# Kernel optimization log

Hardware: AMD Instinct MI355X
Metric: run time of the kernel (lower is better)

## Reference

```python
import jax, jax.numpy as jnp
import numpy as np

EMBED_DIM = 1024
NUM_HEADS = 16
D_K = EMBED_DIM // NUM_HEADS
SCALE = D_K ** -0.5
WEIGHT_EPS = 1e-5


def setup_inputs() -> dict:
    key = jax.random.key(0)
    ks = jax.random.split(key, 12)
    B, T, E = 4, 1024, EMBED_DIM
    init = 1.0 / np.sqrt(E)  # ~ nn.Linear default scale
    inp = {
        "q": jax.random.normal(ks[0], (B, T, E), jnp.float32),
        "k": jax.random.normal(ks[1], (B, T, E), jnp.float32),
        "v": jax.random.normal(ks[2], (B, T, E), jnp.float32),
        "weights": jax.random.uniform(ks[3], (B, T), jnp.float32),
        "Wq": jax.random.uniform(ks[4], (E, E), jnp.float32, -init, init),
        "bq": jax.random.uniform(ks[5], (E,), jnp.float32, -init, init),
        "Wk": jax.random.uniform(ks[6], (E, E), jnp.float32, -init, init),
        "bk": jax.random.uniform(ks[7], (E,), jnp.float32, -init, init),
        "Wv": jax.random.uniform(ks[8], (E, E), jnp.float32, -init, init),
        "bv": jax.random.uniform(ks[9], (E,), jnp.float32, -init, init),
        "Wo": jax.random.uniform(ks[10], (E, E), jnp.float32, -init, init),
        "bo": jax.random.uniform(ks[11], (E,), jnp.float32, -init, init),
    }
    return inp


def reference(q, k, v, weights, Wq, bq, Wk, bk, Wv, bv, Wo, bo):
    B, T, E = q.shape
    H, Dk = NUM_HEADS, D_K
    # linear projections (torch Linear: x @ W.T + b), split into heads
    qh = (q @ Wq.T + bq).reshape(B, T, H, Dk).transpose(0, 2, 1, 3)  # [B,H,T,Dk]
    kh = (k @ Wk.T + bk).reshape(B, T, H, Dk).transpose(0, 2, 1, 3)
    vh = (v @ Wv.T + bv).reshape(B, T, H, Dk).transpose(0, 2, 1, 3)
    # scaled energy [B,H,Tq,Tk]
    energy = jnp.einsum("bhqd,bhkd->bhqk", qh, kh) * SCALE
    # weight^2 gating over key axis + masked_fill(-inf) where weight < eps
    w = weights[:, None, None, :]  # [B,1,1,Tk]
    energy = jnp.where(w < WEIGHT_EPS, -jnp.inf, energy * (w * w))
    attn = jax.nn.softmax(energy, axis=-1)  # dropout is identity in eval mode
    out = jnp.einsum("bhqk,bhkd->bhqd", attn, vh)  # [B,H,T,Dk]
    out = out.transpose(0, 2, 1, 3).reshape(B, T, E)
    return out @ Wo.T + bo
```

## Files before the change

### kernel.cpp

```cpp
#include <hip/hip_runtime.h>
#include <hip/hip_bf16.h>
#include <stdint.h>

using frag = __attribute__((ext_vector_type(8))) short;
using f4   = __attribute__((ext_vector_type(4))) float;
using bf16 = __hip_bfloat16;

static constexpr float WEPS = 1e-5f;
static constexpr float SC2K  = 0.125f * 1.44269504f;
static constexpr float EBIAS = -8.0f * 1.44269504f;

#define AS1(p) ((const __attribute__((address_space(1))) void*)(p))
#define AS3(p) ((__attribute__((address_space(3))) void*)(p))

__device__ __forceinline__ void gl2lds16(const void* g, void* l) {
    __builtin_amdgcn_global_load_lds(AS1(g), AS3(l), 16, 0, 0);
}

__device__ inline uint4 pack8(float4 a, float4 b) {
    union { bf16 h[8]; uint4 u; } x;
    x.h[0] = __float2bfloat16(a.x); x.h[1] = __float2bfloat16(a.y);
    x.h[2] = __float2bfloat16(a.z); x.h[3] = __float2bfloat16(a.w);
    x.h[4] = __float2bfloat16(b.x); x.h[5] = __float2bfloat16(b.y);
    x.h[6] = __float2bfloat16(b.z); x.h[7] = __float2bfloat16(b.w);
    return x.u;
}

__device__ __forceinline__ uint2 pack4(float a, float b, float c, float d) {
    union { bf16 h[4]; uint2 u; } x;
    x.h[0] = __float2bfloat16(a); x.h[1] = __float2bfloat16(b);
    x.h[2] = __float2bfloat16(c); x.h[3] = __float2bfloat16(d);
    return x.u;
}

__device__ __forceinline__ int tperm(int t) {
    return (t & ~63) | (((t & 15) << 2) | ((t >> 4) & 3));
}

struct CvtArgs {
    const float* src[7];
    long long    bounds[8];
    long long    total;
};

__global__ __launch_bounds__(256) void cvt_kernel(CvtArgs a, bf16* __restrict__ dst)
{
    long long e = ((long long)blockIdx.x * 256 + threadIdx.x) * 8;
    if (e >= a.total) return;
    int s = 0;
    while (e >= a.bounds[s + 1]) s++;
    const float* src = a.src[s] + (e - a.bounds[s]);
    float4 f0 = ((const float4*)src)[0];
    float4 f1 = ((const float4*)src)[1];
    *(uint4*)(dst + e) = pack8(f0, f1);
}

struct GemmBatch {
    const void*  A[3];
    const void*  W[3];
    const float* bias[3];
    void*        Out[3];
    int          mode[3];
};

template<bool ABF, bool WBF>
__global__ __launch_bounds__(256) void gemm_batch(GemmBatch g)
{
    constexpr int K = 1024;
    __shared__ bf16 As[128 * 32];
    __shared__ bf16 Bs[128 * 32];

    const int z = blockIdx.z;
    const void*  Ap   = g.A[z];
    const void*  Wp   = g.W[z];
    const float* bias = g.bias[z];
    void*        OutP = g.Out[z];
    const int    mode = g.mode[z];

    const int tid  = threadIdx.x;
    int m0, n0;
    if (mode == 4) { m0 = blockIdx.x * 128; n0 = blockIdx.y * 128; }
    else           { n0 = blockIdx.x * 128; m0 = blockIdx.y * 128; }
    const int lane = tid & 63;
    const int wave = tid >> 6;
    const int wm   = (wave >> 1) * 64;
    const int wn   = (wave & 1) * 64;
    const int lr   = lane & 15;
    const int q    = lane >> 4;

    const int sr = tid >> 1;
    const int sc = (tid & 1) * 16;

    const int c0 = wave * 128 + lane;
    const int c1 = c0 + 64;
    const int r0 = c0 >> 2, col0 = (c0 & 3) * 8;
    const int r1 = c1 >> 2, col1 = (c1 & 3) * 8;

    f4 acc[4][4];
    #pragma unroll
    for (int i = 0; i < 4; i++)
        #pragma unroll
        for (int j = 0; j < 4; j++) acc[i][j] = f4{0.f, 0.f, 0.f, 0.f};

    for (int k0 = 0; k0 < K; k0 += 32) {
        if (WBF) {
            const bf16* W = (const bf16*)Wp;
            gl2lds16(&W[(size_t)(n0 + r0) * K + k0 + col0], &Bs[wave * 1024]);
            gl2lds16(&W[(size_t)(n0 + r1) * K + k0 + col1], &Bs[wave * 1024 + 512]);
        } else {
            const float* W = (const float*)Wp;
            const float* src = &W[(size_t)(n0 + sr) * K + k0 + sc];
            float4 f0 = ((const float4*)src)[0];
            float4 f1 = ((const float4*)src)[1];
            float4 f2 = ((const float4*)src)[2];
            float4 f3 = ((const float4*)src)[3];
            *(uint4*)(&Bs[sr * 32 + sc])     = pack8(f0, f1);
            *(uint4*)(&Bs[sr * 32 + sc + 8]) = pack8(f2, f3);
        }
        if (ABF) {
            const bf16* A = (const bf16*)Ap;
            gl2lds16(&A[(size_t)(m0 + r0) * K + k0 + col0], &As[wave * 1024]);
            gl2lds16(&A[(size_t)(m0 + r1) * K + k0 + col1], &As[wave * 1024 + 512]);
        } else {
            const float* A = (const float*)Ap;
            const float* src = &A[(size_t)(m0 + sr) * K + k0 + sc];
            float4 f0 = ((const float4*)src)[0];
            float4 f1 = ((const float4*)src)[1];
            float4 f2 = ((const float4*)src)[2];
            float4 f3 = ((const float4*)src)[3];
            *(uint4*)(&As[sr * 32 + sc])     = pack8(f0, f1);
            *(uint4*)(&As[sr * 32 + sc + 8]) = pack8(f2, f3);
        }
        __syncthreads();

        frag af[4], bfr[4];
        #pragma unroll
        for (int i = 0; i < 4; i++)
            af[i] = *(const frag*)(&As[(wm + i * 16 + lr) * 32 + q * 8]);
        #pragma unroll
        for (int j = 0; j < 4; j++)
            bfr[j] = *(const frag*)(&Bs[(wn + j * 16 + lr) * 32 + q * 8]);
        #pragma unroll
        for (int i = 0; i < 4; i++)
            #pragma unroll
            for (int j = 0; j < 4; j++)
                acc[i][j] = __builtin_amdgcn_mfma_f32_16x16x32_bf16(af[i], bfr[j], acc[i][j], 0, 0, 0);
        __syncthreads();
    }

    #pragma unroll
    for (int i = 0; i < 4; i++) {
        int row0 = m0 + wm + i * 16 + q * 4;
        if (mode == 4) {
            float bvr[4];
            #pragma unroll
            for (int r = 0; r < 4; r++) bvr[r] = bias[row0 + r];
            #pragma unroll
            for (int j = 0; j < 4; j++) {
                int tok = n0 + wn + j * 16 + lr;
                int bbt = tok >> 10, tt = tperm(tok & 1023);
                #pragma unroll
                for (int r = 0; r < 4; r++) {
                    int f = row0 + r;
                    int h = f >> 6, d = f & 63;
                    float val = acc[i][j][r] + bvr[r];
                    ((bf16*)OutP)[((((size_t)bbt * 16 + h) * 64 + d) << 10) + tt] = __float2bfloat16(val);
                }
            }
        } else {
            #pragma unroll
            for (int j = 0; j < 4; j++) {
                int col = n0 + wn + j * 16 + lr;
                float bv = bias[col];
                #pragma unroll
                for (int r = 0; r < 4; r++) {
                    float val = acc[i][j][r] + bv;
                    int mrow = row0 + r;
                    if (mode == 3) {
                        ((float*)OutP)[(size_t)mrow * 1024 + col] = val;
                    } else {
                        int bb = mrow >> 10, t = mrow & 1023;
                        int h  = col >> 6,   d = col & 63;
                        size_t idx;
                        if (mode == 2)
                            idx = ((((size_t)bb * 16 + h) * 64 + d) << 10) + tperm(t);
                        else
                            idx = ((((size_t)bb * 16 + h) << 10) + t) * 64 + d;
                        ((bf16*)OutP)[idx] = __float2bfloat16(val);
                    }
                }
            }
        }
    }
}

template<bool WBF>
__global__ __launch_bounds__(256) void gemm_out(const bf16* __restrict__ A,
                                                const void* __restrict__ Wp,
                                                const float* __restrict__ bias,
                                                float* __restrict__ Out)
{
    constexpr int K = 1024;
    __shared__ bf16 As[64 * 32];
    __shared__ bf16 Bs[128 * 32];

    const int tid  = threadIdx.x;
    const int n0   = blockIdx.x * 128;
    const int m0   = blockIdx.y * 64;
    const int lane = tid & 63;
    const int wave = tid >> 6;
    const int wm   = (wave >> 1) * 32;
    const int wn   = (wave & 1) * 64;
    const int lr   = lane & 15;
    const int q    = lane >> 4;

    const int sr = tid >> 1;
    const int sc = (tid & 1) * 16;

    const int c0 = wave * 128 + lane;
    const int c1 = c0 + 64;
    const int r0 = c0 >> 2, col0 = (c0 & 3) * 8;
    const int r1 = c1 >> 2, col1 = (c1 & 3) * 8;
    const int ca = wave * 64 + lane;
    const int ra = ca >> 2, cola = (ca & 3) * 8;

    f4 acc[2][4];
    #pragma unroll
    for (int i = 0; i < 2; i++)
        #pragma unroll
        for (int j = 0; j < 4; j++) acc[i][j] = f4{0.f, 0.f, 0.f, 0.f};

    for (int k0 = 0; k0 < K; k0 += 32) {
        if (WBF) {
            const bf16* W = (const bf16*)Wp;
            gl2lds16(&W[(size_t)(n0 + r0) * K + k0 + col0], &Bs[wave * 1024]);
            gl2lds16(&W[(size_t)(n0 + r1) * K + k0 + col1], &Bs[wave * 1024 + 512]);
        } else {
            const float* W = (const float*)Wp;
            const float* src = &W[(size_t)(n0 + sr) * K + k0 + sc];
            float4 f0 = ((const float4*)src)[0];
            float4 f1 = ((const float4*)src)[1];
            float4 f2 = ((const float4*)src)[2];
            float4 f3 = ((const float4*)src)[3];
            *(uint4*)(&Bs[sr * 32 + sc])     = pack8(f0, f1);
            *(uint4*)(&Bs[sr * 32 + sc + 8]) = pack8(f2, f3);
        }
        gl2lds16(&A[(size_t)(m0 + ra) * K + k0 + cola], &As[wave * 512]);
        __syncthreads();

        frag af[2], bfr[4];
        #pragma unroll
        for (int i = 0; i < 2; i++)
            af[i] = *(const frag*)(&As[(wm + i * 16 + lr) * 32 + q * 8]);
        #pragma unroll
        for (int j = 0; j < 4; j++)
            bfr[j] = *(const frag*)(&Bs[(wn + j * 16 + lr) * 32 + q * 8]);
        #pragma unroll
        for (int i = 0; i < 2; i++)
            #pragma unroll
            for (int j = 0; j < 4; j++)
                acc[i][j] = __builtin_amdgcn_mfma_f32_16x16x32_bf16(af[i], bfr[j], acc[i][j], 0, 0, 0);
        __syncthreads();
    }

    #pragma unroll
    for (int i = 0; i < 2; i++) {
        int row0 = m0 + wm + i * 16 + q * 4;
        #pragma unroll
        for (int j = 0; j < 4; j++) {
            int col = n0 + wn + j * 16 + lr;
            float bv = bias[col];
            #pragma unroll
            for (int r = 0; r < 4; r++)
                Out[(size_t)(row0 + r) * 1024 + col] = acc[i][j][r] + bv;
        }
    }
}

__global__ __launch_bounds__(256) void attn_kernel(const bf16* __restrict__ qh,
                                                   const bf16* __restrict__ kh,
                                                   const bf16* __restrict__ vhT,
                                                   const float* __restrict__ wts,
                                                   bf16* __restrict__ att)
{
    __shared__ bf16 Ks[2][64 * 64];
    __shared__ bf16 Vs[2][64 * 64];
    __shared__ bf16 Plds[4][16 * 64];

    const int tid  = threadIdx.x;
    const int lane = tid & 63;
    const int wave = tid >> 6;
    const int lr   = lane & 15;
    const int q    = lane >> 4;
    const int bh   = blockIdx.x;
    const int bb   = bh >> 4;
    const int h    = bh & 15;
    const int q0   = blockIdx.y * 64 + wave * 16;
    const size_t base = (size_t)bh * 1024 * 64;

    const int cA = wave * 128 + lane;
    const int cB = cA + 64;
    const int rowA = cA >> 3, gA = ((cA & 7) ^ (rowA & 7)) * 8;
    const int rowB = cB >> 3, gB = ((cB & 7) ^ (rowB & 7)) * 8;

    frag aq[2];
    #pragma unroll
    for (int ks = 0; ks < 2; ks++)
        aq[ks] = *(const frag*)(&qh[base + (size_t)(q0 + lr) * 64 + ks * 32 + q * 8]);

    float rs[4] = {0.f, 0.f, 0.f, 0.f};
    f4 o[4];
    #pragma unroll
    for (int j = 0; j < 4; j++) o[j] = f4{0.f, 0.f, 0.f, 0.f};

    gl2lds16(&kh [base + (size_t)rowA * 64 + gA],   &Ks[0][wave * 1024]);
    gl2lds16(&kh [base + (size_t)rowB * 64 + gB],   &Ks[0][wave * 1024 + 512]);
    gl2lds16(&vhT[base + (size_t)rowA * 1024 + gA], &Vs[0][wave * 1024]);
    gl2lds16(&vhT[base + (size_t)rowB * 1024 + gB], &Vs[0][wave * 1024 + 512]);
    __syncthreads();

    for (int t = 0; t < 16; t++) {
        const int k0  = t * 64;
        const int buf = t & 1;
        if (t < 15) {
            int kn = k0 + 64;
            gl2lds16(&kh [base + (size_t)(kn + rowA) * 64 + gA],  &Ks[buf ^ 1][wave * 1024]);
            gl2lds16(&kh [base + (size_t)(kn + rowB) * 64 + gB],  &Ks[buf ^ 1][wave * 1024 + 512]);
            gl2lds16(&vhT[base + (size_t)rowA * 1024 + kn + gA], &Vs[buf ^ 1][wave * 1024]);
            gl2lds16(&vhT[base + (size_t)rowB * 1024 + kn + gB], &Vs[buf ^ 1][wave * 1024 + 512]);
        }

        float sc2[4], eb[4];
        #pragma unroll
        for (int j = 0; j < 4; j++) {
            float w = wts[bb * 1024 + k0 + j * 16 + lr];
            sc2[j] = SC2K * w * w;
            eb[j]  = (w < WEPS) ? -1e30f : EBIAS;
        }

        f4 s[4];
        #pragma unroll
        for (int j = 0; j < 4; j++) {
            int rowj = j * 16 + lr;
            int s0 = ((q    ) ^ (rowj & 7)) * 8;
            int s1 = ((q + 4) ^ (rowj & 7)) * 8;
            frag b0 = *(const frag*)(&Ks[buf][rowj * 64 + s0]);
            frag b1 = *(const frag*)(&Ks[buf][rowj * 64 + s1]);
            f4 z = f4{0.f, 0.f, 0.f, 0.f};
            s[j] = __builtin_amdgcn_mfma_f32_16x16x32_bf16(aq[0], b0, z, 0, 0, 0);
            s[j] = __builtin_amdgcn_mfma_f32_16x16x32_bf16(aq[1], b1, s[j], 0, 0, 0);
        }

        float p[4][4];
        #pragma unroll
        for (int j = 0; j < 4; j++)
            #pragma unroll
            for (int r = 0; r < 4; r++) {
                p[j][r] = __builtin_amdgcn_exp2f(fmaf(s[j][r], sc2[j], eb[j]));
                rs[r] += p[j][r];
            }
        #pragma unroll
        for (int r = 0; r < 4; r++)
            *(uint2*)(&Plds[wave][(q * 4 + r) * 64 + lr * 4]) =
                pack4(p[0][r], p[1][r], p[2][r], p[3][r]);

        frag ap[2];
        #pragma unroll
        for (int ks = 0; ks < 2; ks++)
            ap[ks] = *(const frag*)(&Plds[wave][lr * 64 + ks * 32 + q * 8]);

        #pragma unroll
        for (int j = 0; j < 4; j++) {
            int rowj = j * 16 + lr;
            int s0 = ((q    ) ^ (rowj & 7)) * 8;
            int s1 = ((q + 4) ^ (rowj & 7)) * 8;
            frag v0 = *(const frag*)(&Vs[buf][rowj * 64 + s0]);
            frag v1 = *(const frag*)(&Vs[buf][rowj * 64 + s1]);
            o[j] = __builtin_amdgcn_mfma_f32_16x16x32_bf16(ap[0], v0, o[j], 0, 0, 0);
            o[j] = __builtin_amdgcn_mfma_f32_16x16x32_bf16(ap[1], v1, o[j], 0, 0, 0);
        }
        __syncthreads();
    }

    #pragma unroll
    for (int off = 1; off < 16; off <<= 1)
        #pragma unroll
        for (int r = 0; r < 4; r++)
            rs[r] += __shfl_xor(rs[r], off, 64);
    float inv[4];
    #pragma unroll
    for (int r = 0; r < 4; r++) inv[r] = 1.0f / rs[r];

    const int t0 = q0 + q * 4;
    #pragma unroll
    for (int j = 0; j < 4; j++) {
        int d = h * 64 + j * 16 + lr;
        #pragma unroll
        for (int r = 0; r < 4; r++)
            att[((size_t)bb * 1024 + t0 + r) * 1024 + d] =
                __float2bfloat16(o[j][r] * inv[r]);
    }
}

extern "C" void kernel_launch(void* const* d_in, const int* in_sizes, int n_in,
                              void* d_out, int out_size, void* d_ws, size_t ws_size,
                              hipStream_t stream)
{
    const float* q   = (const float*)d_in[0];
    const float* k   = (const float*)d_in[1];
    const float* v   = (const float*)d_in[2];
    const float* wts = (const float*)d_in[3];
    const float* Wq  = (const float*)d_in[4];
    const float* bq  = (const float*)d_in[5];
    const float* Wk  = (const float*)d_in[6];
    const float* bk  = (const float*)d_in[7];
    const float* Wv  = (const float*)d_in[8];
    const float* bv  = (const float*)d_in[9];
    const float* Wo  = (const float*)d_in[10];
    const float* bo  = (const float*)d_in[11];
    float* out = (float*)d_out;

    const long long Mi = 1024 * 1024;
    bf16* qh  = (bf16*)d_ws;
    bf16* kh  = qh  + 4 * Mi;
    bf16* vhT = kh  + 4 * Mi;
    bf16* att = vhT + 4 * Mi;
    bf16* cvt = att + 4 * Mi;
    const size_t base_bytes = (size_t)32 * Mi;

    dim3 blk(256);

    if (ws_size >= base_bytes + (size_t)32 * Mi) {
        CvtArgs ca{};
        ca.src[0] = q;  ca.src[1] = k;  ca.src[2] = v;
        ca.src[3] = Wq; ca.src[4] = Wk; ca.src[5] = Wv; ca.src[6] = Wo;
        long long bnd[8] = {0, 4*Mi, 8*Mi, 12*Mi, 13*Mi, 14*Mi, 15*Mi, 16*Mi};
        for (int i = 0; i < 8; i++) ca.bounds[i] = bnd[i];
        ca.total = 16 * Mi;
        cvt_kernel<<<8192, blk, 0, stream>>>(ca, cvt);

        GemmBatch gq{};
        gq.A[0] = cvt;          gq.A[1] = cvt + 4*Mi;   gq.A[2] = cvt + 14*Mi;
        gq.W[0] = cvt + 12*Mi;  gq.W[1] = cvt + 13*Mi;  gq.W[2] = cvt + 8*Mi;
        gq.bias[0] = bq; gq.bias[1] = bk; gq.bias[2] = bv;
        gq.Out[0] = qh;  gq.Out[1] = kh;  gq.Out[2] = vhT;
        gq.mode[0] = 0;  gq.mode[1] = 0;  gq.mode[2] = 4;
        gemm_batch<true, true><<<dim3(8, 32, 3), blk, 0, stream>>>(gq);

        attn_kernel<<<dim3(64, 16), blk, 0, stream>>>(qh, kh, vhT, wts, att);

        gemm_out<true><<<dim3(8, 64), blk, 0, stream>>>(att, cvt + 15*Mi, bo, out);
    } else if (ws_size >= base_bytes + (size_t)8 * Mi) {
        CvtArgs ca{};
        ca.src[0] = Wq; ca.src[1] = Wk; ca.src[2] = Wv; ca.src[3] = Wo;
        long long bnd[8] = {0, 1*Mi, 2*Mi, 3*Mi, 4*Mi, 4*Mi, 4*Mi, 4*Mi};
        for (int i = 0; i < 8; i++) ca.bounds[i] = bnd[i];
        ca.total = 4 * Mi;
        cvt_kernel<<<2048, blk, 0, stream>>>(ca, cvt);

        GemmBatch gq{};
        gq.A[0] = q; gq.A[1] = k; gq.A[2] = v;
        gq.W[0] = cvt; gq.W[1] = cvt + 1*Mi; gq.W[2] = cvt + 2*Mi;
        gq.bias[0] = bq; gq.bias[1] = bk; gq.bias[2] = bv;
        gq.Out[0] = qh;  gq.Out[1] = kh;  gq.Out[2] = vhT;
        gq.mode[0] = 0;  gq.mode[1] = 0;  gq.mode[2] = 2;
        gemm_batch<false, true><<<dim3(8, 32, 3), blk, 0, stream>>>(gq);

        attn_kernel<<<dim3(64, 16), blk, 0, stream>>>(qh, kh, vhT, wts, att);

        gemm_out<true><<<dim3(8, 64), blk, 0, stream>>>(att, cvt + 3*Mi, bo, out);
    } else {
        GemmBatch gq{};
        gq.A[0] = q; gq.A[1] = k; gq.A[2] = v;
        gq.W[0] = Wq; gq.W[1] = Wk; gq.W[2] = Wv;
        gq.bias[0] = bq; gq.bias[1] = bk; gq.bias[2] = bv;
        gq.Out[0] = qh;  gq.Out[1] = kh;  gq.Out[2] = vhT;
        gq.mode[0] = 0;  gq.mode[1] = 0;  gq.mode[2] = 2;
        gemm_batch<false, false><<<dim3(8, 32, 3), blk, 0, stream>>>(gq);

        attn_kernel<<<dim3(64, 16), blk, 0, stream>>>(qh, kh, vhT, wts, att);

        gemm_out<false><<<dim3(8, 64), blk, 0, stream>>>(att, Wo, bo, out);
    }
}
```

Baseline: 226.6 us.

## Double query rows per attention wave and vectorize transposed V stores

The attention kernel now gives each wave 32 query rows as two 16-row fragments instead of one, so each K and V tile read from LDS feeds twice as many MFMAs, and the grid's query dimension is halved. The P staging buffer is padded to a 72-element row pitch to reduce LDS bank conflicts. The projection GEMM's transposed-V epilogue now packs four bf16 values into one 8-byte store in place of scalar scattered stores, and both kernels get a launch-bounds occupancy hint of 3. This raises register pressure and halves the number of attention blocks. The packed store also assumes tperm leaves four adjacent tokens contiguous, since it is no longer applied per token.

```diff
diff --git a/kernel.cpp b/kernel.cpp
--- a/kernel.cpp
+++ b/kernel.cpp
@@ -64,7 +64,7 @@
 };
 
 template<bool ABF, bool WBF>
-__global__ __launch_bounds__(256) void gemm_batch(GemmBatch g)
+__global__ __launch_bounds__(256, 3) void gemm_batch(GemmBatch g)
 {
     constexpr int K = 1024;
     __shared__ bf16 As[128 * 32];
@@ -148,26 +148,27 @@
         __syncthreads();
     }
 
-    #pragma unroll
-    for (int i = 0; i < 4; i++) {
-        int row0 = m0 + wm + i * 16 + q * 4;
-        if (mode == 4) {
-            float bvr[4];
-            #pragma unroll
-            for (int r = 0; r < 4; r++) bvr[r] = bias[row0 + r];
-            #pragma unroll
-            for (int j = 0; j < 4; j++) {
-                int tok = n0 + wn + j * 16 + lr;
-                int bbt = tok >> 10, tt = tperm(tok & 1023);
-                #pragma unroll
-                for (int r = 0; r < 4; r++) {
-                    int f = row0 + r;
-                    int h = f >> 6, d = f & 63;
-                    float val = acc[i][j][r] + bvr[r];
-                    ((bf16*)OutP)[((((size_t)bbt * 16 + h) * 64 + d) << 10) + tt] = __float2bfloat16(val);
-                }
+    if (mode == 4) {
+        const int bbt   = (n0 + wn) >> 10;
+        const int tbase = (n0 + wn) & 1023;
+        bf16* O = (bf16*)OutP;
+        #pragma unroll
+        for (int i = 0; i < 4; i++) {
+            int row0 = m0 + wm + i * 16 + q * 4;
+            #pragma unroll
+            for (int r = 0; r < 4; r++) {
+                int f = row0 + r;
+                int h = f >> 6, d = f & 63;
+                float bv = bias[f];
+                size_t idx = ((((size_t)bbt * 16 + h) * 64 + d) << 10) + tbase + lr * 4;
+                *(uint2*)(&O[idx]) = pack4(acc[i][0][r] + bv, acc[i][1][r] + bv,
+                                           acc[i][2][r] + bv, acc[i][3][r] + bv);
             }
-        } else {
+        }
+    } else {
+        #pragma unroll
+        for (int i = 0; i < 4; i++) {
+            int row0 = m0 + wm + i * 16 + q * 4;
             #pragma unroll
             for (int j = 0; j < 4; j++) {
                 int col = n0 + wn + j * 16 + lr;
@@ -277,15 +278,16 @@
     }
 }
 
-__global__ __launch_bounds__(256) void attn_kernel(const bf16* __restrict__ qh,
-                                                   const bf16* __restrict__ kh,
-                                                   const bf16* __restrict__ vhT,
-                                                   const float* __restrict__ wts,
-                                                   bf16* __restrict__ att)
+__global__ __launch_bounds__(256, 3) void attn_kernel(const bf16* __restrict__ qh,
+                                                      const bf16* __restrict__ kh,
+                                                      const bf16* __restrict__ vhT,
+                                                      const float* __restrict__ wts,
+                                                      bf16* __restrict__ att)
 {
+    constexpr int LDP = 72;
     __shared__ bf16 Ks[2][64 * 64];
     __shared__ bf16 Vs[2][64 * 64];
-    __shared__ bf16 Plds[4][16 * 64];
+    __shared__ bf16 Plds[4][32 * LDP];
 
     const int tid  = threadIdx.x;
     const int lane = tid & 63;
@@ -295,7 +297,7 @@
     const int bh   = blockIdx.x;
     const int bb   = bh >> 4;
     const int h    = bh & 15;
-    const int q0   = blockIdx.y * 64 + wave * 16;
+    const int q0w  = blockIdx.y * 128 + wave * 32;
     const size_t base = (size_t)bh * 1024 * 64;
 
     const int cA = wave * 128 + lane;
@@ -303,15 +305,22 @@
     const int rowA = cA >> 3, gA = ((cA & 7) ^ (rowA & 7)) * 8;
     const int rowB = cB >> 3, gB = ((cB & 7) ^ (rowB & 7)) * 8;
 
-    frag aq[2];
-    #pragma unroll
-    for (int ks = 0; ks < 2; ks++)
-        aq[ks] = *(const frag*)(&qh[base + (size_t)(q0 + lr) * 64 + ks * 32 + q * 8]);
-
-    float rs[4] = {0.f, 0.f, 0.f, 0.f};
-    f4 o[4];
-    #pragma unroll
-    for (int j = 0; j < 4; j++) o[j] = f4{0.f, 0.f, 0.f, 0.f};
+    frag aq[2][2];
+    #pragma unroll
+    for (int rf = 0; rf < 2; rf++)
+        #pragma unroll
+        for (int ks = 0; ks < 2; ks++)
+            aq[rf][ks] = *(const frag*)(&qh[base + (size_t)(q0w + rf * 16 + lr) * 64 + ks * 32 + q * 8]);
+
+    float rs[2][4];
+    f4 o[2][4];
+    #pragma unroll
+    for (int rf = 0; rf < 2; rf++)
+        #pragma unroll
+        for (int j = 0; j < 4; j++) {
+            o[rf][j] = f4{0.f, 0.f, 0.f, 0.f};
+            rs[rf][j] = 0.f;
+        }
 
     gl2lds16(&kh [base + (size_t)rowA * 64 + gA],   &Ks[0][wave * 1024]);
     gl2lds16(&kh [base + (size_t)rowB * 64 + gB],   &Ks[0][wave * 1024 + 512]);
@@ -338,46 +347,54 @@
             eb[j]  = (w < WEPS) ? -1e30f : EBIAS;
         }
 
-        f4 s[4];
+        frag kb[4][2];
         #pragma unroll
         for (int j = 0; j < 4; j++) {
             int rowj = j * 16 + lr;
-            int s0 = ((q    ) ^ (rowj & 7)) * 8;
-            int s1 = ((q + 4) ^ (rowj & 7)) * 8;
-            frag b0 = *(const frag*)(&Ks[buf][rowj * 64 + s0]);
-            frag b1 = *(const frag*)(&Ks[buf][rowj * 64 + s1]);
-            f4 z = f4{0.f, 0.f, 0.f, 0.f};
-            s[j] = __builtin_amdgcn_mfma_f32_16x16x32_bf16(aq[0], b0, z, 0, 0, 0);
-            s[j] = __builtin_amdgcn_mfma_f32_16x16x32_bf16(aq[1], b1, s[j], 0, 0, 0);
-        }
-
-        float p[4][4];
-        #pragma unroll
-        for (int j = 0; j < 4; j++)
-            #pragma unroll
-            for (int r = 0; r < 4; r++) {
-                p[j][r] = __builtin_amdgcn_exp2f(fmaf(s[j][r], sc2[j], eb[j]));
-                rs[r] += p[j][r];
+            kb[j][0] = *(const frag*)(&Ks[buf][rowj * 64 + (((q    ) ^ (rowj & 7)) * 8)]);
+            kb[j][1] = *(const frag*)(&Ks[buf][rowj * 64 + (((q + 4) ^ (rowj & 7)) * 8)]);
+        }
+
+        #pragma unroll
+        for (int rf = 0; rf < 2; rf++) {
+            f4 s[4];
+            #pragma unroll
+            for (int j = 0; j < 4; j++) {
+                f4 z = f4{0.f, 0.f, 0.f, 0.f};
+                s[j] = __builtin_amdgcn_mfma_f32_16x16x32_bf16(aq[rf][0], kb[j][0], z, 0, 0, 0);
+                s[j] = __builtin_amdgcn_mfma_f32_16x16x32_bf16(aq[rf][1], kb[j][1], s[j], 0, 0, 0);
             }
-        #pragma unroll
-        for (int r = 0; r < 4; r++)
-            *(uint2*)(&Plds[wave][(q * 4 + r) * 64 + lr * 4]) =
-                pack4(p[0][r], p[1][r], p[2][r], p[3][r]);
-
-        frag ap[2];
-        #pragma unroll
-        for (int ks = 0; ks < 2; ks++)
-            ap[ks] = *(const frag*)(&Plds[wave][lr * 64 + ks * 32 + q * 8]);
-
+            float p[4][4];
+            #pragma unroll
+            for (int j = 0; j < 4; j++)
+                #pragma unroll
+                for (int r = 0; r < 4; r++) {
+                    p[j][r] = __builtin_amdgcn_exp2f(fmaf(s[j][r], sc2[j], eb[j]));
+                    rs[rf][r] += p[j][r];
+                }
+            #pragma unroll
+            for (int r = 0; r < 4; r++)
+                *(uint2*)(&Plds[wave][(rf * 16 + q * 4 + r) * LDP + lr * 4]) =
+                    pack4(p[0][r], p[1][r], p[2][r], p[3][r]);
+        }
+
+        frag vb[4][2];
         #pragma unroll
         for (int j = 0; j < 4; j++) {
             int rowj = j * 16 + lr;
-            int s0 = ((q    ) ^ (rowj & 7)) * 8;
-            int s1 = ((q + 4) ^ (rowj & 7)) * 8;
-            frag v0 = *(const frag*)(&Vs[buf][rowj * 64 + s0]);
-            frag v1 = *(const frag*)(&Vs[buf][rowj * 64 + s1]);
-            o[j] = __builtin_amdgcn_mfma_f32_16x16x32_bf16(ap[0], v0, o[j], 0, 0, 0);
-            o[j] = __builtin_amdgcn_mfma_f32_16x16x32_bf16(ap[1], v1, o[j], 0, 0, 0);
+            vb[j][0] = *(const frag*)(&Vs[buf][rowj * 64 + (((q    ) ^ (rowj & 7)) * 8)]);
+            vb[j][1] = *(const frag*)(&Vs[buf][rowj * 64 + (((q + 4) ^ (rowj & 7)) * 8)]);
+        }
+
+        #pragma unroll
+        for (int rf = 0; rf < 2; rf++) {
+            frag ap0 = *(const frag*)(&Plds[wave][(rf * 16 + lr) * LDP + q * 8]);
+            frag ap1 = *(const frag*)(&Plds[wave][(rf * 16 + lr) * LDP + 32 + q * 8]);
+            #pragma unroll
+            for (int j = 0; j < 4; j++) {
+                o[rf][j] = __builtin_amdgcn_mfma_f32_16x16x32_bf16(ap0, vb[j][0], o[rf][j], 0, 0, 0);
+                o[rf][j] = __builtin_amdgcn_mfma_f32_16x16x32_bf16(ap1, vb[j][1], o[rf][j], 0, 0, 0);
+            }
         }
         __syncthreads();
     }
@@ -385,20 +402,25 @@
     #pragma unroll
     for (int off = 1; off < 16; off <<= 1)
         #pragma unroll
-        for (int r = 0; r < 4; r++)
-            rs[r] += __shfl_xor(rs[r], off, 64);
-    float inv[4];
-    #pragma unroll
-    for (int r = 0; r < 4; r++) inv[r] = 1.0f / rs[r];
-
-    const int t0 = q0 + q * 4;
-    #pragma unroll
-    for (int j = 0; j < 4; j++) {
-        int d = h * 64 + j * 16 + lr;
-        #pragma unroll
-        for (int r = 0; r < 4; r++)
-            att[((size_t)bb * 1024 + t0 + r) * 1024 + d] =
-                __float2bfloat16(o[j][r] * inv[r]);
+        for (int rf = 0; rf < 2; rf++)
+            #pragma unroll
+            for (int r = 0; r < 4; r++)
+                rs[rf][r] += __shfl_xor(rs[rf][r], off, 64);
+
+    #pragma unroll
+    for (int rf = 0; rf < 2; rf++) {
+        float inv[4];
+        #pragma unroll
+        for (int r = 0; r < 4; r++) inv[r] = 1.0f / rs[rf][r];
+        const int t0 = q0w + rf * 16 + q * 4;
+        #pragma unroll
+        for (int j = 0; j < 4; j++) {
+            int d = h * 64 + j * 16 + lr;
+            #pragma unroll
+            for (int r = 0; r < 4; r++)
+                att[((size_t)bb * 1024 + t0 + r) * 1024 + d] =
+                    __float2bfloat16(o[rf][j][r] * inv[r]);
+        }
     }
 }
 
@@ -447,7 +469,7 @@
         gq.mode[0] = 0;  gq.mode[1] = 0;  gq.mode[2] = 4;
         gemm_batch<true, true><<<dim3(8, 32, 3), blk, 0, stream>>>(gq);
 
-        attn_kernel<<<dim3(64, 16), blk, 0, stream>>>(qh, kh, vhT, wts, att);
+        attn_kernel<<<dim3(64, 8), blk, 0, stream>>>(qh, kh, vhT, wts, att);
 
         gemm_out<true><<<dim3(8, 64), blk, 0, stream>>>(att, cvt + 15*Mi, bo, out);
     } else if (ws_size >= base_bytes + (size_t)8 * Mi) {
@@ -466,7 +488,7 @@
         gq.mode[0] = 0;  gq.mode[1] = 0;  gq.mode[2] = 2;
         gemm_batch<false, true><<<dim3(8, 32, 3), blk, 0, stream>>>(gq);
 
-        attn_kernel<<<dim3(64, 16), blk, 0, stream>>>(qh, kh, vhT, wts, att);
+        attn_kernel<<<dim3(64, 8), blk, 0, stream>>>(qh, kh, vhT, wts, att);
 
         gemm_out<true><<<dim3(8, 64), blk, 0, stream>>>(att, cvt + 3*Mi, bo, out);
     } else {
@@ -478,7 +500,7 @@
         gq.mode[0] = 0;  gq.mode[1] = 0;  gq.mode[2] = 2;
         gemm_batch<false, false><<<dim3(8, 32, 3), blk, 0, stream>>>(gq);
 
-        attn_kernel<<<dim3(64, 16), blk, 0, stream>>>(qh, kh, vhT, wts, att);
+        attn_kernel<<<dim3(64, 8), blk, 0, stream>>>(qh, kh, vhT, wts, att);
 
         gemm_out<false><<<dim3(8, 64), blk, 0, stream>>>(att, Wo, bo, out);
     }
```

Measured after the change: 214.1 us. 5.5% less time.
